# Optimization experiments

Measured on AMD Instinct MI355X. Metric: run time of the kernel, lower is better.

Reference implementation:

```python
import jax, jax.numpy as jnp
import numpy as np

D = 43           # d_model for '80k'
H1 = 30          # dense1
H2 = 20          # dense2
FEAT = 8


def _lstm_dir(x, w_ih, w_hh, b_ih, b_hh, reverse):
    # x: [B, T, I]; w_ih: [4H, I]; w_hh: [4H, H]; PyTorch gate order i,f,g,o
    B = x.shape[0]
    H = w_hh.shape[1]
    xs = jnp.swapaxes(x, 0, 1)                 # [T, B, I]
    b = b_ih + b_hh
    xz = xs @ w_ih.T + b                        # precompute input GEMM: [T, B, 4H]

    def step(carry, zt):
        h, c = carry
        z = zt + h @ w_hh.T
        i, f, g, o = jnp.split(z, 4, axis=-1)
        i = jax.nn.sigmoid(i); f = jax.nn.sigmoid(f)
        g = jnp.tanh(g);       o = jax.nn.sigmoid(o)
        c = f * c + i * g
        h = o * jnp.tanh(c)
        return (h, c), h

    h0 = jnp.zeros((B, H), x.dtype)
    _, hs = jax.lax.scan(step, (h0, h0), xz, reverse=reverse)
    return jnp.swapaxes(hs, 0, 1)               # [B, T, H]


def _bilstm(x, wf, wb):
    fwd = _lstm_dir(x, *wf, reverse=False)
    bwd = _lstm_dir(x, *wb, reverse=True)
    return jnp.concatenate([fwd, bwd], axis=-1)  # [B, T, 2H]


def setup_inputs() -> dict:
    key = jax.random.key(0)
    ks = iter(jax.random.split(key, 32))
    s = 0.1
    def rn(shape):
        return (jax.random.normal(next(ks), shape, dtype=jnp.float32) * s)
    inp = {"x": jax.random.normal(next(ks), (256, 2048, FEAT), dtype=jnp.float32)}
    # input projection (LazyLinear -> Linear(FEAT, D))
    inp["w_proj"] = rn((D, FEAT)); inp["b_proj"] = rn((D,))
    # lstm1: input D, hidden D, bidirectional
    for tag, isz in (("1f", D), ("1b", D), ("2f", 2 * D), ("2b", 2 * D)):
        inp[f"w_ih{tag}"] = rn((4 * D, isz))
        inp[f"w_hh{tag}"] = rn((4 * D, D))
        inp[f"b_ih{tag}"] = rn((4 * D,))
        inp[f"b_hh{tag}"] = rn((4 * D,))
    inp["w_d1"] = rn((H1, 2 * D)); inp["b_d1"] = rn((H1,))
    inp["w_d2"] = rn((H2, H1));    inp["b_d2"] = rn((H2,))
    inp["w_out"] = rn((1, H2));    inp["b_out"] = rn((1,))
    return inp


def reference(x, w_proj, b_proj,
              w_ih1f, w_hh1f, b_ih1f, b_hh1f,
              w_ih1b, w_hh1b, b_ih1b, b_hh1b,
              w_ih2f, w_hh2f, b_ih2f, b_hh2f,
              w_ih2b, w_hh2b, b_ih2b, b_hh2b,
              w_d1, b_d1, w_d2, b_d2, w_out, b_out):
    h = x @ w_proj.T + b_proj                                   # [B,T,D]
    h = _bilstm(h, (w_ih1f, w_hh1f, b_ih1f, b_hh1f),
                   (w_ih1b, w_hh1b, b_ih1b, b_hh1b))            # [B,T,2D]
    h = _bilstm(h, (w_ih2f, w_hh2f, b_ih2f, b_hh2f),
                   (w_ih2b, w_hh2b, b_ih2b, b_hh2b))            # [B,T,2D]
    h = jax.nn.relu(h @ w_d1.T + b_d1)
    h = jax.nn.relu(h @ w_d2.T + b_d2)
    return h @ w_out.T + b_out                                  # [B,T,1]
```

## Files before the change

### kernel.cpp

```cpp
#include <hip/hip_runtime.h>
#include <hip/hip_bf16.h>
#include <math.h>

#define DD   43
#define TT   2048
#define BB   256
#define FEAT 8
#define MB   16
#define NPAD 192
#define NH1  30
#define NH2  20

using bf16 = __hip_bfloat16;
typedef __attribute__((ext_vector_type(8))) short bf16x8;
typedef __attribute__((ext_vector_type(4))) int   i32x4;
typedef __attribute__((ext_vector_type(4))) float f32x4;

__device__ __forceinline__ float ldv(const float* p) { return *p; }
__device__ __forceinline__ float ldv(const bf16* p)  { return __bfloat162float(*p); }

__device__ __forceinline__ short f2b(float f) {
    bf16 h = __float2bfloat16(f);
    return *reinterpret_cast<short*>(&h);
}
#define LOG2E 1.44269504f
__device__ __forceinline__ float sig_(float x) {
    return __builtin_amdgcn_rcpf(1.0f + __builtin_amdgcn_exp2f(-LOG2E * x));
}
__device__ __forceinline__ float tanh_(float x) {
    return fmaf(-2.0f, __builtin_amdgcn_rcpf(1.0f + __builtin_amdgcn_exp2f(2.0f * LOG2E * x)), 1.0f);
}
__device__ __forceinline__ bf16x8 mk8(const unsigned u[4]) {
    union { unsigned u[4]; bf16x8 v; } x;
    x.u[0] = u[0]; x.u[1] = u[1]; x.u[2] = u[2]; x.u[3] = u[3];
    return x.v;
}
__device__ __forceinline__ void mfma_a(f32x4& d, bf16x8 a, i32x4 b) {
    asm("v_mfma_f32_16x16x32_bf16 %0, %1, %2, %0" : "+v"(d) : "v"(a), "a"(b));
}

__global__ void prep_kernel(
    const float* __restrict__ wp, const float* __restrict__ bp,
    const float* __restrict__ w_ih1f, const float* __restrict__ w_hh1f,
    const float* __restrict__ b_ih1f, const float* __restrict__ b_hh1f,
    const float* __restrict__ w_ih1b, const float* __restrict__ w_hh1b,
    const float* __restrict__ b_ih1b, const float* __restrict__ b_hh1b,
    const float* __restrict__ w_ih2f, const float* __restrict__ w_hh2f,
    const float* __restrict__ b_ih2f, const float* __restrict__ b_hh2f,
    const float* __restrict__ w_ih2b, const float* __restrict__ w_hh2b,
    const float* __restrict__ b_ih2b, const float* __restrict__ b_hh2b,
    short* __restrict__ W1, short* __restrict__ W2,
    float* __restrict__ bias1, float* __restrict__ bias2)
{
    const int KP1 = 96, KP2 = 160;
    const int S1 = 2 * NPAD * KP1, S2 = 2 * NPAD * KP2, S3 = 2 * NPAD;
    int idx = blockIdx.x * blockDim.x + threadIdx.x;
    if (idx < S1) {
        int dir = idx / (NPAD * KP1), rem = idx % (NPAD * KP1);
        int n = rem / KP1, k = rem % KP1;
        int q = n / 48, dq = n % 48;
        float v = 0.0f;
        if (dq < DD) {
            int orig = q * DD + dq;
            const float* wih = dir ? w_ih1b : w_ih1f;
            const float* whh = dir ? w_hh1b : w_hh1f;
            if (k < FEAT) {
                for (int d = 0; d < DD; ++d) v = fmaf(wih[orig * DD + d], wp[d * FEAT + k], v);
            } else if (k >= 32 && k < 32 + DD) {
                v = whh[orig * DD + (k - 32)];
            }
        }
        W1[idx] = f2b(v);
    } else if (idx < S1 + S2) {
        int j = idx - S1;
        int dir = j / (NPAD * KP2), rem = j % (NPAD * KP2);
        int n = rem / KP2, k = rem % KP2;
        int q = n / 48, dq = n % 48;
        float v = 0.0f;
        if (dq < DD) {
            int orig = q * DD + dq;
            const float* wih = dir ? w_ih2b : w_ih2f;
            const float* whh = dir ? w_hh2b : w_hh2f;
            if (k < 2 * DD)                  v = wih[orig * (2 * DD) + k];
            else if (k >= 96 && k < 96 + DD) v = whh[orig * DD + (k - 96)];
        }
        W2[j] = f2b(v);
    } else if (idx < S1 + S2 + S3) {
        int j = idx - S1 - S2;
        int dir = j / NPAD, n = j % NPAD;
        int q = n / 48, dq = n % 48;
        float v = 0.0f;
        if (dq < DD) {
            int orig = q * DD + dq;
            const float* wih = dir ? w_ih1b : w_ih1f;
            const float* bi  = dir ? b_ih1b : b_ih1f;
            const float* bh  = dir ? b_hh1b : b_hh1f;
            v = bi[orig] + bh[orig];
            for (int d = 0; d < DD; ++d) v = fmaf(wih[orig * DD + d], bp[d], v);
        }
        bias1[j] = v;
    } else if (idx < S1 + S2 + 2 * S3) {
        int j = idx - S1 - S2 - S3;
        int dir = j / NPAD, n = j % NPAD;
        int q = n / 48, dq = n % 48;
        float v = 0.0f;
        if (dq < DD) {
            int orig = q * DD + dq;
            const float* bi = dir ? b_ih2b : b_ih2f;
            const float* bh = dir ? b_hh2b : b_hh2f;
            v = bi[orig] + bh[orig];
        }
        bias2[j] = v;
    }
}

template <int KSX, bool XRAW>
__global__ __launch_bounds__(192, 1)
void lstm_mfma(
    const void*  __restrict__ in_,
    const short* __restrict__ Wb,
    const float* __restrict__ bias,
    bf16* __restrict__ out)
{
    constexpr int KS   = KSX + 2;
    constexpr int KPAD = KS * 32;

    const int dir   = blockIdx.x & 1;
    const int btile = blockIdx.x >> 1;
    const int tid   = threadIdx.x;
    const int lane  = tid & 63;
    const int wv    = tid >> 6;
    const int ln15  = lane & 15;
    const int lg    = lane >> 4;

    __shared__ __align__(16) short hbuf[2][MB][72];

    const int  dq   = wv * 16 + ln15;
    const bool dval = dq < DD;

    i32x4 wx[4][KSX];
    i32x4 wh[4][2];
    float bv[4];
    {
        const short* Wd = Wb + (size_t)dir * NPAD * KPAD;
#pragma unroll
        for (int q = 0; q < 4; ++q) {
            const short* row = Wd + (size_t)(q * 48 + dq) * KPAD;
#pragma unroll
            for (int ks = 0; ks < KSX; ++ks)
                wx[q][ks] = *reinterpret_cast<const i32x4*>(row + ks * 32 + lg * 8);
            wh[q][0] = *reinterpret_cast<const i32x4*>(row + KSX * 32 + lg * 8);
            wh[q][1] = *reinterpret_cast<const i32x4*>(row + (KSX + 1) * 32 + lg * 8);
            bv[q] = bias[dir * NPAD + q * 48 + dq];
        }
#pragma unroll
        for (int q = 0; q < 4; ++q) {
#pragma unroll
            for (int ks = 0; ks < KSX; ++ks)
                asm volatile("" : "+a"(wx[q][ks]));
            asm volatile("" : "+a"(wh[q][0]), "+a"(wh[q][1]));
        }
    }

    for (int i = tid; i < 2 * MB * 72; i += 192) ((short*)hbuf)[i] = 0;

    const long t0  = dir ? (TT - 1) : 0;
    const int  stp = dir ? -1 : 1;
    const int  bb  = btile * MB + ln15;

    unsigned xe[KSX][4], xo[KSX][4];
    auto load_x = [&](long t, unsigned (&xf)[KSX][4]) {
        long tc = t < 0 ? 0 : (t >= TT ? TT - 1 : t);
        if constexpr (XRAW) {
            if (lg == 0) {
                const float* xp = (const float*)in_ + ((long)bb * TT + tc) * FEAT;
                float4 v0 = *reinterpret_cast<const float4*>(xp);
                float4 v1 = *reinterpret_cast<const float4*>(xp + 4);
                xf[0][0] = ((unsigned)(unsigned short)f2b(v0.y) << 16) | (unsigned short)f2b(v0.x);
                xf[0][1] = ((unsigned)(unsigned short)f2b(v0.w) << 16) | (unsigned short)f2b(v0.z);
                xf[0][2] = ((unsigned)(unsigned short)f2b(v1.y) << 16) | (unsigned short)f2b(v1.x);
                xf[0][3] = ((unsigned)(unsigned short)f2b(v1.w) << 16) | (unsigned short)f2b(v1.z);
            } else {
#pragma unroll
                for (int j = 0; j < 4; ++j) xf[0][j] = 0u;
            }
        } else {
            const short* xp = (const short*)in_ + ((long)bb * TT + tc) * (2 * DD);
#pragma unroll
            for (int ks = 0; ks < KSX; ++ks)
#pragma unroll
                for (int j = 0; j < 4; ++j) {
                    int k = ks * 32 + lg * 8 + 2 * j;
                    xf[ks][j] = (k < 2 * DD) ? *reinterpret_cast<const unsigned*>(xp + k) : 0u;
                }
        }
    };

    auto xinit = [&](unsigned (&xf)[KSX][4], f32x4 (&xa)[4]) {
#pragma unroll
        for (int q = 0; q < 4; ++q) {
            f32x4 a = {bv[q], bv[q], bv[q], bv[q]};
#pragma unroll
            for (int ks = 0; ks < KSX; ++ks)
                mfma_a(a, mk8(xf[ks]), wx[q][ks]);
            xa[q] = a;
        }
    };

    float cc[4] = {0.0f, 0.0f, 0.0f, 0.0f};
    f32x4 xaccE[4], xaccO[4];

    load_x(t0, xe);
    load_x(t0 + stp, xo);
    __syncthreads();
    xinit(xe, xaccE);

    auto step = [&](unsigned (&cur)[KSX][4], unsigned (&oth)[KSX][4],
                    f32x4 (&accC)[4], f32x4 (&accN)[4], int par, long t) {
        bf16x8 ah0 = *reinterpret_cast<const bf16x8*>(&hbuf[par][ln15][lg * 8]);
        bf16x8 ah1 = *reinterpret_cast<const bf16x8*>(&hbuf[par][ln15][32 + lg * 8]);
#pragma unroll
        for (int q = 0; q < 4; ++q) {
            mfma_a(accC[q], ah0, wh[q][0]);
            mfma_a(accC[q], ah1, wh[q][1]);
        }
        load_x(t + 2 * stp, cur);
        xinit(oth, accN);

#pragma unroll
        for (int r = 0; r < 4; ++r) {
            float ig = sig_(accC[0][r]);
            float fg = sig_(accC[1][r]);
            float gg = tanh_(accC[2][r]);
            float og = sig_(accC[3][r]);
            cc[r] = fmaf(fg, cc[r], ig * gg);
            float h = og * tanh_(cc[r]);
            if (dval) {
                hbuf[par ^ 1][lg * 4 + r][dq] = f2b(h);
                out[((long)(btile * MB + lg * 4 + r) * TT + t) * (2 * DD) + dir * DD + dq] =
                    __float2bfloat16(h);
            }
        }
        asm volatile("s_waitcnt lgkmcnt(0)" ::: "memory");
        __builtin_amdgcn_sched_barrier(0);
        __builtin_amdgcn_s_barrier();
    };

    long t = t0;
    for (int s = 0; s < TT; s += 2) {
        step(xe, xo, xaccE, xaccO, 0, t); t += stp;
        step(xo, xe, xaccO, xaccE, 1, t); t += stp;
    }
}

template <typename TIN>
__global__ void head_kernel(const TIN* __restrict__ h2,
                            const float* __restrict__ w1, const float* __restrict__ b1,
                            const float* __restrict__ w2, const float* __restrict__ b2,
                            const float* __restrict__ w3, const float* __restrict__ b3,
                            float* __restrict__ outp) {
    long bt = (long)blockIdx.x * blockDim.x + threadIdx.x;
    if (bt >= (long)BB * TT) return;
    float v[2 * DD];
    const TIN* src = h2 + bt * (2 * DD);
#pragma unroll
    for (int k = 0; k < 2 * DD; ++k) v[k] = ldv(&src[k]);

    float m1[NH1];
#pragma unroll
    for (int j = 0; j < NH1; ++j) {
        float a = b1[j];
        const float* w = w1 + j * (2 * DD);
#pragma unroll
        for (int k = 0; k < 2 * DD; ++k) a = fmaf(w[k], v[k], a);
        m1[j] = fmaxf(a, 0.0f);
    }
    float m2[NH2];
#pragma unroll
    for (int j = 0; j < NH2; ++j) {
        float a = b2[j];
        const float* w = w2 + j * NH1;
#pragma unroll
        for (int k = 0; k < NH1; ++k) a = fmaf(w[k], m1[k], a);
        m2[j] = fmaxf(a, 0.0f);
    }
    float a = b3[0];
#pragma unroll
    for (int k = 0; k < NH2; ++k) a = fmaf(w3[k], m2[k], a);
    outp[bt] = a;
}

extern "C" void kernel_launch(void* const* d_in, const int* in_sizes, int n_in,
                              void* d_out, int out_size, void* d_ws, size_t ws_size,
                              hipStream_t stream) {
    const float* x      = (const float*)d_in[0];
    const float* w_proj = (const float*)d_in[1];
    const float* b_proj = (const float*)d_in[2];
    const float* w_ih1f = (const float*)d_in[3];
    const float* w_hh1f = (const float*)d_in[4];
    const float* b_ih1f = (const float*)d_in[5];
    const float* b_hh1f = (const float*)d_in[6];
    const float* w_ih1b = (const float*)d_in[7];
    const float* w_hh1b = (const float*)d_in[8];
    const float* b_ih1b = (const float*)d_in[9];
    const float* b_hh1b = (const float*)d_in[10];
    const float* w_ih2f = (const float*)d_in[11];
    const float* w_hh2f = (const float*)d_in[12];
    const float* b_ih2f = (const float*)d_in[13];
    const float* b_hh2f = (const float*)d_in[14];
    const float* w_ih2b = (const float*)d_in[15];
    const float* w_hh2b = (const float*)d_in[16];
    const float* b_ih2b = (const float*)d_in[17];
    const float* b_hh2b = (const float*)d_in[18];
    const float* w_d1   = (const float*)d_in[19];
    const float* b_d1   = (const float*)d_in[20];
    const float* w_d2   = (const float*)d_in[21];
    const float* b_d2   = (const float*)d_in[22];
    const float* w_out  = (const float*)d_in[23];
    const float* b_out  = (const float*)d_in[24];
    (void)in_sizes; (void)n_in; (void)out_size; (void)ws_size;

    char* wsb = (char*)d_ws;
    short* W1    = (short*)(wsb);
    short* W2    = (short*)(wsb + 73728);
    float* bias1 = (float*)(wsb + 73728 + 122880);
    float* bias2 = (float*)(wsb + 73728 + 122880 + 1536);
    const size_t o_big = 262144;
    const size_t n1    = (size_t)BB * TT * 2 * DD;
    bf16* out1 = (bf16*)(wsb + o_big);
    bf16* out2 = (bf16*)(wsb + o_big + n1 * sizeof(bf16));

    {
        const int total = 2 * NPAD * 96 + 2 * NPAD * 160 + 2 * (2 * NPAD);
        prep_kernel<<<(total + 255) / 256, 256, 0, stream>>>(
            w_proj, b_proj,
            w_ih1f, w_hh1f, b_ih1f, b_hh1f, w_ih1b, w_hh1b, b_ih1b, b_hh1b,
            w_ih2f, w_hh2f, b_ih2f, b_hh2f, w_ih2b, w_hh2b, b_ih2b, b_hh2b,
            W1, W2, bias1, bias2);
    }
    lstm_mfma<1, true><<<2 * (BB / MB), 192, 0, stream>>>(x, W1, bias1, out1);
    lstm_mfma<3, false><<<2 * (BB / MB), 192, 0, stream>>>(out1, W2, bias2, out2);
    head_kernel<bf16><<<(int)(((long)BB * TT + 255) / 256), 256, 0, stream>>>(
        out2, w_d1, b_d1, w_d2, b_d2, w_out, b_out, (float*)d_out);
}
```

Baseline: 3.616 ms.

## Stage LSTM outputs in LDS and write padded 88-wide rows in 8-step bursts

Each LSTM direction now writes its hidden states into a shared-memory tile covering 8 timesteps, then flushes the tile to global memory as 8-byte vector stores. This replaces the per-element scattered 2-byte stores done every step. The intermediate buffer is padded to 88 columns, so each direction gets a 44-wide slot. Layer-2 weights and the head kernel's reads are remapped to skip the padding column. The change adds LDS usage, a periodic flush pass after the barrier, and a somewhat larger intermediate buffer.

```diff
diff --git a/kernel.cpp b/kernel.cpp
--- a/kernel.cpp
+++ b/kernel.cpp
@@ -8,6 +8,7 @@
 #define FEAT 8
 #define MB   16
 #define NPAD 192
+#define ROWS 88
 #define NH1  30
 #define NH2  20
 
@@ -15,6 +16,7 @@
 typedef __attribute__((ext_vector_type(8))) short bf16x8;
 typedef __attribute__((ext_vector_type(4))) int   i32x4;
 typedef __attribute__((ext_vector_type(4))) float f32x4;
+typedef __attribute__((ext_vector_type(2))) unsigned u32x2;
 
 __device__ __forceinline__ float ldv(const float* p) { return *p; }
 __device__ __forceinline__ float ldv(const bf16* p)  { return __bfloat162float(*p); }
@@ -81,8 +83,9 @@
             int orig = q * DD + dq;
             const float* wih = dir ? w_ih2b : w_ih2f;
             const float* whh = dir ? w_hh2b : w_hh2f;
-            if (k < 2 * DD)                  v = wih[orig * (2 * DD) + k];
-            else if (k >= 96 && k < 96 + DD) v = whh[orig * DD + (k - 96)];
+            if (k < DD)                        v = wih[orig * (2 * DD) + k];
+            else if (k >= 44 && k < 44 + DD)   v = wih[orig * (2 * DD) + (k - 1)];
+            else if (k >= 96 && k < 96 + DD)   v = whh[orig * DD + (k - 96)];
         }
         W2[j] = f2b(v);
     } else if (idx < S1 + S2 + S3) {
@@ -120,7 +123,7 @@
     const void*  __restrict__ in_,
     const short* __restrict__ Wb,
     const float* __restrict__ bias,
-    bf16* __restrict__ out)
+    short* __restrict__ out)
 {
     constexpr int KS   = KSX + 2;
     constexpr int KPAD = KS * 32;
@@ -134,6 +137,7 @@
     const int lg    = lane >> 4;
 
     __shared__ __align__(16) short hbuf[2][MB][72];
+    __shared__ __align__(16) short tile[2][8][MB][44];
 
     const int  dq   = wv * 16 + ln15;
     const bool dval = dq < DD;
@@ -167,13 +171,14 @@
     const long t0  = dir ? (TT - 1) : 0;
     const int  stp = dir ? -1 : 1;
     const int  bb  = btile * MB + ln15;
+    const int  bt0 = btile * MB;
 
     unsigned xe[KSX][4], xo[KSX][4];
     auto load_x = [&](long t, unsigned (&xf)[KSX][4]) {
         long tc = t < 0 ? 0 : (t >= TT ? TT - 1 : t);
         if constexpr (XRAW) {
             if (lg == 0) {
-                const float* xp = (const float*)in_ + ((long)bb * TT + tc) * FEAT;
+                const float* xp = (const float*)in_ + ((size_t)bb * TT + tc) * FEAT;
                 float4 v0 = *reinterpret_cast<const float4*>(xp);
                 float4 v1 = *reinterpret_cast<const float4*>(xp + 4);
                 xf[0][0] = ((unsigned)(unsigned short)f2b(v0.y) << 16) | (unsigned short)f2b(v0.x);
@@ -185,14 +190,17 @@
                 for (int j = 0; j < 4; ++j) xf[0][j] = 0u;
             }
         } else {
-            const short* xp = (const short*)in_ + ((long)bb * TT + tc) * (2 * DD);
-#pragma unroll
-            for (int ks = 0; ks < KSX; ++ks)
+            const short* xp = (const short*)in_ + ((size_t)bb * TT + tc) * ROWS;
+#pragma unroll
+            for (int ks = 0; ks < KSX; ++ks) {
+                int k0 = ks * 32 + lg * 8;
 #pragma unroll
                 for (int j = 0; j < 4; ++j) {
-                    int k = ks * 32 + lg * 8 + 2 * j;
-                    xf[ks][j] = (k < 2 * DD) ? *reinterpret_cast<const unsigned*>(xp + k) : 0u;
+                    unsigned v = 0u;
+                    if (k0 < ROWS) v = *reinterpret_cast<const unsigned*>(xp + k0 + 2 * j);
+                    xf[ks][j] = v;
                 }
+            }
         }
     };
 
@@ -216,7 +224,7 @@
     xinit(xe, xaccE);
 
     auto step = [&](unsigned (&cur)[KSX][4], unsigned (&oth)[KSX][4],
-                    f32x4 (&accC)[4], f32x4 (&accN)[4], int par, long t) {
+                    f32x4 (&accC)[4], f32x4 (&accN)[4], int par, int s, long t) {
         bf16x8 ah0 = *reinterpret_cast<const bf16x8*>(&hbuf[par][ln15][lg * 8]);
         bf16x8 ah1 = *reinterpret_cast<const bf16x8*>(&hbuf[par][ln15][32 + lg * 8]);
 #pragma unroll
@@ -227,6 +235,8 @@
         load_x(t + 2 * stp, cur);
         xinit(oth, accN);
 
+        const int ti = (int)(t & 7);
+        short* tw = &tile[(s >> 3) & 1][ti][lg * 4][0];
 #pragma unroll
         for (int r = 0; r < 4; ++r) {
             float ig = sig_(accC[0][r]);
@@ -235,37 +245,53 @@
             float og = sig_(accC[3][r]);
             cc[r] = fmaf(fg, cc[r], ig * gg);
             float h = og * tanh_(cc[r]);
-            if (dval) {
-                hbuf[par ^ 1][lg * 4 + r][dq] = f2b(h);
-                out[((long)(btile * MB + lg * 4 + r) * TT + t) * (2 * DD) + dir * DD + dq] =
-                    __float2bfloat16(h);
-            }
+            short hb = f2b(h);
+            if (dval) hbuf[par ^ 1][lg * 4 + r][dq] = hb;
+            if (dq < 44) tw[r * 44 + dq] = hb;
         }
         asm volatile("s_waitcnt lgkmcnt(0)" ::: "memory");
         __builtin_amdgcn_sched_barrier(0);
         __builtin_amdgcn_s_barrier();
+
+        if ((s & 7) == 7) {
+            const short* tp = &tile[(s >> 3) & 1][0][0][0];
+            long tbase = t & ~7L;
+#pragma unroll
+            for (int i = 0; i < 8; ++i) {
+                int c = i * 192 + tid;
+                if (c < 128 * 11) {
+                    int row = c / 11, sub = c - row * 11;
+                    int tr = row >> 4, b = row & 15;
+                    u32x2 v = *reinterpret_cast<const u32x2*>(tp + row * 44 + sub * 4);
+                    *reinterpret_cast<u32x2*>(
+                        out + ((size_t)(bt0 + b) * TT + (tbase + tr)) * ROWS
+                            + dir * 44 + sub * 4) = v;
+                }
+            }
+        }
     };
 
     long t = t0;
     for (int s = 0; s < TT; s += 2) {
-        step(xe, xo, xaccE, xaccO, 0, t); t += stp;
-        step(xo, xe, xaccO, xaccE, 1, t); t += stp;
-    }
-}
-
-template <typename TIN>
-__global__ void head_kernel(const TIN* __restrict__ h2,
+        step(xe, xo, xaccE, xaccO, 0, s, t);     t += stp;
+        step(xo, xe, xaccO, xaccE, 1, s + 1, t); t += stp;
+    }
+}
+
+__global__ void head_kernel(const short* __restrict__ h2,
                             const float* __restrict__ w1, const float* __restrict__ b1,
                             const float* __restrict__ w2, const float* __restrict__ b2,
                             const float* __restrict__ w3, const float* __restrict__ b3,
                             float* __restrict__ outp) {
     long bt = (long)blockIdx.x * blockDim.x + threadIdx.x;
     if (bt >= (long)BB * TT) return;
+    const bf16* src = (const bf16*)(h2 + (size_t)bt * ROWS);
     float v[2 * DD];
-    const TIN* src = h2 + bt * (2 * DD);
-#pragma unroll
-    for (int k = 0; k < 2 * DD; ++k) v[k] = ldv(&src[k]);
-
+#pragma unroll
+    for (int k = 0; k < 2 * DD; ++k) {
+        int kp = (k < DD) ? k : k + 1;
+        v[k] = ldv(&src[kp]);
+    }
     float m1[NH1];
 #pragma unroll
     for (int j = 0; j < NH1; ++j) {
@@ -325,10 +351,10 @@
     short* W2    = (short*)(wsb + 73728);
     float* bias1 = (float*)(wsb + 73728 + 122880);
     float* bias2 = (float*)(wsb + 73728 + 122880 + 1536);
-    const size_t o_big = 262144;
-    const size_t n1    = (size_t)BB * TT * 2 * DD;
-    bf16* out1 = (bf16*)(wsb + o_big);
-    bf16* out2 = (bf16*)(wsb + o_big + n1 * sizeof(bf16));
+    const size_t o_big  = 262144;
+    const size_t lay_sz = (size_t)BB * TT * ROWS * sizeof(short);
+    short* out1 = (short*)(wsb + o_big);
+    short* out2 = (short*)(wsb + o_big + lay_sz);
 
     {
         const int total = 2 * NPAD * 96 + 2 * NPAD * 160 + 2 * (2 * NPAD);
@@ -340,6 +366,6 @@
     }
     lstm_mfma<1, true><<<2 * (BB / MB), 192, 0, stream>>>(x, W1, bias1, out1);
     lstm_mfma<3, false><<<2 * (BB / MB), 192, 0, stream>>>(out1, W2, bias2, out2);
-    head_kernel<bf16><<<(int)(((long)BB * TT + 255) / 256), 256, 0, stream>>>(
+    head_kernel<<<(int)(((long)BB * TT + 255) / 256), 256, 0, stream>>>(
         out2, w_d1, b_d1, w_d2, b_d2, w_out, b_out, (float*)d_out);
 }
```

Result: slower. 3.935 ms (+8.8%).
